# Performance work log

Measured on AMD Instinct MI355X. Metric: run time of the kernel, lower is better.

Reference implementation:

```python
import jax, jax.numpy as jnp
import numpy as np

PI = 3.1415927410125732
N = 4096
L = 1.28e-3          # box side [m]
VEL = 5e-7
RC = 3.15e-6         # Rc = diameter/2
RR = 8e-6
RO = 2.5e-5
RA = np.inf
DT_TRANS = 1.4e-14   # DT (translational diffusion)
DR = 0.0028
GAMMA = 25.0
DT = 0.2             # timestep dt
COLL_ITERS = 30      # fixed cap for collision-resolution do-while (orig caps at 1000)


def setup_inputs() -> dict:
    key = jax.random.key(0)
    ks = jax.random.split(key, 7)
    pos_re = jax.random.uniform(ks[0], (N,), jnp.float32) * L
    pos_im = jax.random.uniform(ks[1], (N,), jnp.float32) * L
    ang = jax.random.uniform(ks[2], (N,), jnp.float32, -PI, PI)
    ori_re = jnp.cos(ang)
    ori_im = jnp.sin(ang)
    deltas = jax.random.uniform(ks[3], (N,), jnp.float32) * 0.5
    rot_noise = jax.random.normal(ks[4], (N,), jnp.float32)
    tn_re = jax.random.normal(ks[5], (N,), jnp.float32)
    tn_im = jax.random.normal(ks[6], (N,), jnp.float32)
    return {"pos_re": pos_re, "pos_im": pos_im, "ori_re": ori_re, "ori_im": ori_im,
            "deltas": deltas, "rot_noise": rot_noise, "tn_re": tn_re, "tn_im": tn_im}


def _wrap(diff):
    # torch get_anglediff wrap: (-2pi,2pi) -> ~(-pi,pi)
    diff = jnp.where(diff <= -PI, jnp.mod(diff, PI), diff)
    return diff - (diff >= PI).astype(diff.dtype) * (2.0 * PI)


def _anglediff(a, b):
    return _wrap(jnp.angle(a) - jnp.angle(b))


def _cossim(a, b):
    # nn.CosineSimilarity(dim=1, eps=1e-14) on view_as_real vectors
    dot = a.real * b.real + a.imag * b.imag
    na = jnp.maximum(jnp.abs(a), 1e-14)
    nb = jnp.maximum(jnp.abs(b), 1e-14)
    return dot / (na * nb)


def _mvc(W, z):
    # real [n,n] mask @ complex [n] vector
    return W @ z.real + 1j * (W @ z.imag)


def _solve_collisions(pos):
    n = pos.shape[0]
    eye_f = jnp.eye(n, dtype=jnp.float32)
    eye_c = eye_f.astype(pos.dtype)

    def step(p):
        diff = p[None, :] - p[:, None] + eye_c  # [i,j] = pos_j - pos_i; diag dummy 1 (nan-safe)
        absd = jnp.abs(diff)
        coll = absd <= (2.0 * RC - eye_f)       # diag threshold negative -> self excluded
        move = jnp.where(coll, diff / jnp.where(coll, absd, 1.0) * ((2.1 * RC - absd) * 0.5), 0.0)
        return p - move.sum(axis=1), coll.sum()

    def body(carry, _):
        p, cont = carry
        p_new, ncoll = step(p)
        p = jnp.where(cont, p_new, p)           # do-while: apply move, then continue if collisions
        return (p, jnp.logical_and(cont, ncoll > 0)), None

    body = jax.checkpoint(body)
    (pos, _), _ = jax.lax.scan(body, (pos, jnp.array(True)), None, length=COLL_ITERS)
    return pos


def _forward(pos_re, pos_im, ori_re, ori_im, deltas, rot_noise, tn_re, tn_im):
    pos = (pos_re + 1j * pos_im).astype(jnp.complex64)
    ori = (ori_re + 1j * ori_im).astype(jnp.complex64)
    n = pos.shape[0]
    eye_b = jnp.eye(n, dtype=bool)

    # pairwise |pos_i - pos_j|; diag made 1 to keep abs() grad-safe (diag is masked out / re-added below)
    dists = jnp.abs(pos[:, None] - pos[None, :] + jnp.eye(n, dtype=pos.dtype))
    mask_rr = (dists <= RR) & ~eye_b              # repulsion zone, self excluded (eye subtracted in orig)
    mask_ro = (dists <= RO + RC) | eye_b          # orientation zone, self included (diag dist 0 in orig)
    mask_ra = (dists <= RA + RC) | eye_b          # Ra = inf -> all ones

    # alpha == 2*pi exactly -> within_view branch skipped (matches original)
    ang = jnp.angle(ori)
    abs_ad = jnp.abs(_wrap(ang[:, None] - ang[None, :]))
    in_front = abs_ad < PI / 2

    Wrr = (mask_rr & in_front).astype(jnp.float32)
    Wro = mask_ro.astype(jnp.float32)
    Wra = mask_ra.astype(jnp.float32)

    n_r = Wrr.sum(axis=1)
    S = _mvc(Wrr, pos) / jnp.maximum(n_r, 1.0) - pos * jnp.sign(n_r)
    d = -S

    n_a = Wra.sum(axis=1)
    cms = _mvc(Wra, pos) / jnp.maximum(n_a, 1.0)
    Ps = cms - pos * jnp.sign(n_a)

    osum = _mvc(Wro, ori)
    left = Ps * jnp.exp(1j * deltas)
    right = Ps * jnp.exp(-1j * deltas)

    # T (=300) >= T_release (=200): choose best turn by cosine similarity
    best = jnp.where(_cossim(left, osum) >= _cossim(right, osum), left, right)

    has_rep = jnp.abs(d) > 0.0
    d_safe = jnp.where(has_rep, d, jnp.ones_like(d))
    att = jnp.where(has_rep, _anglediff(d_safe, ori), _anglediff(best, ori))

    s2dr = np.float32(np.sqrt(2.0 * DR))
    sdt = np.float32(np.sqrt(DT))
    rot = jnp.exp(1j * (DT * GAMMA * DR * jnp.sin(att) + rot_noise * s2dr * sdt))

    # complex standard normal: real/imag each N(0, 1/sqrt(2))
    tnoise = (tn_re + 1j * tn_im) * np.float32(np.sqrt(0.5)) * np.float32(np.sqrt(2.0 * DT_TRANS))
    trans = DT * VEL * ori + tnoise * sdt

    new_pos = _solve_collisions(pos + trans)
    new_ori = ori * rot

    c2r = lambda z: jnp.stack([z.real, z.imag], axis=-1)
    # [5, N, 2]: positions, orientations, orientation_sums, leftturns, rightturns (real views)
    return jnp.stack([c2r(new_pos), c2r(new_ori), c2r(osum), c2r(left), c2r(right)], axis=0)


def reference(pos_re, pos_im, ori_re, ori_im, deltas, rot_noise, tn_re, tn_im):
    return _forward(pos_re, pos_im, ori_re, ori_im, deltas, rot_noise, tn_re, tn_im)
```

## Files before the change

kernel.cpp:

```cpp
#include <hip/hip_runtime.h>

#define NPART 4096
#define PI_F 3.1415927410125732f
#define TWO_PI_F 6.2831854820251465f
#define SENT 4096

__device__ __forceinline__ float wrapf(float d) {
    if (d <= -PI_F) {
        d = fmodf(d, PI_F);
        if (d < 0.0f) d += PI_F;
    }
    if (d >= PI_F) d -= TWO_PI_F;
    return d;
}

__global__ __launch_bounds__(512)
void k_interact(const float* __restrict__ pr, const float* __restrict__ pim,
                const float* __restrict__ orr, const float* __restrict__ oim,
                const float* __restrict__ deltas,
                const float* __restrict__ rot_noise,
                const float* __restrict__ tn_re, const float* __restrict__ tn_im,
                float* __restrict__ out,
                uint2* __restrict__ recQuad, int* __restrict__ recC,
                unsigned short* __restrict__ recNbr16) {
    constexpr float RR_F  = 8e-6f;
    constexpr float RR2   = RR_F * RR_F;
    constexpr float ROC_F = (float)(2.5e-5 + 3.15e-6);
    constexpr float ROC2  = ROC_F * ROC_F;
    constexpr float CUT_F = 14.3e-6f;
    constexpr float CUT2  = CUT_F * CUT_F;

    __shared__ float2 lsP[512];
    __shared__ float2 lsO[512];
    __shared__ float rA0[512], rA1[512], rA2[512], rA3[512], rA4[512];
    __shared__ float rB0[512], rB1[512], rB2[512], rB3[512], rB4[512];
    __shared__ float cr_[512], ci_[512];
    __shared__ int ncnt[16];
    __shared__ unsigned short nbrL[16 * 16];

    int tid = threadIdx.x;
    int li = tid & 7, sl = tid >> 3;
    int i0 = blockIdx.x * 16 + li;
    int i1 = i0 + 8;

    if (tid < 16) ncnt[tid] = 0;

    float pxA = pr[i0], pyA = pim[i0], oxA = orr[i0], oyA = oim[i0];
    float pxB = pr[i1], pyB = pim[i1], oxB = orr[i1], oyB = oim[i1];

    float nAr = 0.0f, SAre = 0.0f, SAim = 0.0f, oAre = 0.0f, oAim = 0.0f;
    float nBr = 0.0f, SBre = 0.0f, SBim = 0.0f, oBre = 0.0f, oBim = 0.0f;
    float cs_re = 0.0f, cs_im = 0.0f;

    for (int c = 0; c < 8; ++c) {
        int j0 = c * 512;
        __syncthreads();
        float jr = pr[j0 + tid], ji = pim[j0 + tid];
        lsP[tid] = make_float2(jr, ji);
        lsO[tid] = make_float2(orr[j0 + tid], oim[j0 + tid]);
        cs_re += jr; cs_im += ji;
        __syncthreads();
#pragma unroll
        for (int t = 0; t < 8; ++t) {
            int jj = sl * 8 + ((t + sl) & 7);
            int j = j0 + jj;
            float2 pv = lsP[jj];
            float drA = pxA - pv.x, diA = pyA - pv.y;
            float d2A = drA * drA + diA * diA;
            float drB = pxB - pv.x, diB = pyB - pv.y;
            float d2B = drB * drB + diB * diB;
            if (__any((d2A <= ROC2) | (d2B <= ROC2))) {
                float2 ov = lsO[jj];
                if (d2A <= ROC2) { oAre += ov.x; oAim += ov.y; }
                float dotA = oxA * ov.x + oyA * ov.y;
                if ((d2A <= RR2) & (dotA > 0.0f) & (j != i0)) {
                    nAr += 1.0f; SAre += pv.x; SAim += pv.y;
                }
                if (d2A <= CUT2 && j != i0) {
                    int slot = atomicAdd(&ncnt[li], 1);
                    if (slot < 16) nbrL[li * 16 + slot] = (unsigned short)j;
                }
                if (d2B <= ROC2) { oBre += ov.x; oBim += ov.y; }
                float dotB = oxB * ov.x + oyB * ov.y;
                if ((d2B <= RR2) & (dotB > 0.0f) & (j != i1)) {
                    nBr += 1.0f; SBre += pv.x; SBim += pv.y;
                }
                if (d2B <= CUT2 && j != i1) {
                    int slot = atomicAdd(&ncnt[li + 8], 1);
                    if (slot < 16) nbrL[(li + 8) * 16 + slot] = (unsigned short)j;
                }
            }
        }
    }

    rA0[tid] = nAr; rA1[tid] = SAre; rA2[tid] = SAim; rA3[tid] = oAre; rA4[tid] = oAim;
    rB0[tid] = nBr; rB1[tid] = SBre; rB2[tid] = SBim; rB3[tid] = oBre; rB4[tid] = oBim;
    cr_[tid] = cs_re; ci_[tid] = cs_im;
    __syncthreads();
    for (int s = 256; s >= 8; s >>= 1) {
        if (tid < s) {
            rA0[tid] += rA0[tid + s]; rA1[tid] += rA1[tid + s];
            rA2[tid] += rA2[tid + s]; rA3[tid] += rA3[tid + s];
            rA4[tid] += rA4[tid + s];
            rB0[tid] += rB0[tid + s]; rB1[tid] += rB1[tid + s];
            rB2[tid] += rB2[tid + s]; rB3[tid] += rB3[tid + s];
            rB4[tid] += rB4[tid + s];
            cr_[tid] += cr_[tid + s];  ci_[tid] += ci_[tid + s];
        }
        __syncthreads();
    }
    if (tid < 4) { cr_[tid] += cr_[tid + 4]; ci_[tid] += ci_[tid + 4]; }
    __syncthreads();
    if (tid < 2) { cr_[tid] += cr_[tid + 2]; ci_[tid] += ci_[tid + 2]; }
    __syncthreads();
    if (tid == 0) { cr_[0] += cr_[1]; ci_[0] += ci_[1]; }
    __syncthreads();

    if (tid < 16) {
        int i = blockIdx.x * 16 + tid;
        float n_r, S_re, S_im, o_re, o_im, px, py, ox, oy;
        if (tid < 8) {
            n_r = rA0[tid]; S_re = rA1[tid]; S_im = rA2[tid];
            o_re = rA3[tid]; o_im = rA4[tid];
            px = pxA; py = pyA; ox = oxA; oy = oyA;
        } else {
            int g = tid - 8;
            n_r = rB0[g]; S_re = rB1[g]; S_im = rB2[g];
            o_re = rB3[g]; o_im = rB4[g];
            px = pxB; py = pyB; ox = oxB; oy = oyB;
        }

        float maxnr = fmaxf(n_r, 1.0f);
        float sgn = (n_r > 0.0f) ? 1.0f : 0.0f;
        float Sre = S_re / maxnr - px * sgn;
        float Sim = S_im / maxnr - py * sgn;
        float d_re = -Sre, d_im = -Sim;

        float cmsx = cr_[0] * (1.0f / 4096.0f);
        float cmsy = ci_[0] * (1.0f / 4096.0f);
        float Ps_re = cmsx - px;
        float Ps_im = cmsy - py;

        float dl = deltas[i];
        float cd = cosf(dl), sd = sinf(dl);
        float l_re = Ps_re * cd - Ps_im * sd;
        float l_im = Ps_re * sd + Ps_im * cd;
        float r_re = Ps_re * cd + Ps_im * sd;
        float r_im = Ps_im * cd - Ps_re * sd;

        float nb   = fmaxf(hypotf(o_re, o_im), 1e-14f);
        float na_l = fmaxf(hypotf(l_re, l_im), 1e-14f);
        float na_r = fmaxf(hypotf(r_re, r_im), 1e-14f);
        float csl = (l_re * o_re + l_im * o_im) / (na_l * nb);
        float csr = (r_re * o_re + r_im * o_im) / (na_r * nb);
        float b_re = (csl >= csr) ? l_re : r_re;
        float b_im = (csl >= csr) ? l_im : r_im;

        float ai = atan2f(oy, ox);
        bool has_rep = (d_re != 0.0f) || (d_im != 0.0f);
        float att;
        if (has_rep) att = wrapf(atan2f(d_im, d_re) - ai);
        else         att = wrapf(atan2f(b_im, b_re) - ai);

        constexpr float GDD  = (float)(0.2 * 25.0 * 0.0028);
        constexpr float S2DR = 0.07483314773547883f;
        constexpr float SDT  = 0.44721359549995793f;
        float theta = GDD * sinf(att) + (rot_noise[i] * S2DR) * SDT;
        float rr_ = cosf(theta), ri_ = sinf(theta);

        float no_re = ox * rr_ - oy * ri_;
        float no_im = ox * ri_ + oy * rr_;

        constexpr float DTVEL = (float)(0.2 * 5e-7);
        constexpr float C1 = 0.70710678118654752f;
        constexpr float C2 = 1.6733200530681511e-07f;
        float t_re = DTVEL * ox + ((tn_re[i] * C1) * C2) * SDT;
        float t_im = DTVEL * oy + ((tn_im[i] * C1) * C2) * SDT;
        float p0x = px + t_re, p0y = py + t_im;

        float2* o2 = (float2*)out;
        o2[i]            = make_float2(p0x, p0y);
        o2[1 * 4096 + i] = make_float2(no_re, no_im);
        o2[2 * 4096 + i] = make_float2(o_re, o_im);
        o2[3 * 4096 + i] = make_float2(l_re, l_im);
        o2[4 * 4096 + i] = make_float2(r_re, r_im);

        int c = min(ncnt[tid], 16);
        unsigned q0 = (c > 0) ? nbrL[tid * 16 + 0] : (unsigned)SENT;
        unsigned q1 = (c > 1) ? nbrL[tid * 16 + 1] : (unsigned)SENT;
        unsigned q2 = (c > 2) ? nbrL[tid * 16 + 2] : (unsigned)SENT;
        unsigned q3 = (c > 3) ? nbrL[tid * 16 + 3] : (unsigned)SENT;
        recQuad[i] = make_uint2(q0 | (q1 << 16), q2 | (q3 << 16));
        recC[i] = c;
        if (c > 4) {
            int cp = (c + 3) & ~3;
            for (int m = 4; m < cp; ++m)
                recNbr16[i * 16 + m] = (m < c) ? nbrL[tid * 16 + m]
                                               : (unsigned short)SENT;
        }
    }
}

__global__ __launch_bounds__(1024)
void k_coll_all(const uint2* __restrict__ recQuad, const int* __restrict__ recC,
                const unsigned short* __restrict__ recNbr16,
                float* __restrict__ out, int* __restrict__ dbg) {
    constexpr float TWO_RC  = (float)(2.0 * 3.15e-6);
    constexpr float TWO_RC2 = TWO_RC * TWO_RC;
    constexpr float C21RC   = (float)(2.1 * 3.15e-6);

    __shared__ float2 pos[NPART + 2];
    __shared__ __align__(16) unsigned short pool[128 * 16];
    __shared__ int flg[2];
    __shared__ int poolCnt;
    __shared__ unsigned bmp[2][132];

    int tid = threadIdx.x;
    if (tid == 0) {
        pos[SENT] = make_float2(1e9f, 1e9f);
        flg[0] = 0; flg[1] = 0; poolCnt = 0;
    }
    if (tid < 132) { bmp[0][tid] = 0u; bmp[1][tid] = 0u; }

    const float2* o2in = (const float2*)out;
    float myx[4], myy[4];
    int myc[4], myo[4];
    int nq0[4], nq1[4], nq2[4], nq3[4];
    bool pm[4];
#pragma unroll
    for (int s = 0; s < 4; ++s) {
        int i = s * 1024 + tid;
        float2 p = o2in[i];
        myx[s] = p.x; myy[s] = p.y;
        pos[i] = p;
        uint2 q = recQuad[i];
        nq0[s] = q.x & 0xffff; nq1[s] = q.x >> 16;
        nq2[s] = q.y & 0xffff; nq3[s] = q.y >> 16;
        myc[s] = recC[i];
        myo[s] = -1;
        pm[s] = true;
    }
    __syncthreads();

#pragma unroll
    for (int s = 0; s < 4; ++s) {
        if (myc[s] > 4) {
            int r = atomicAdd(&poolCnt, 1);
            if (r < 128) {
                int i = s * 1024 + tid;
                const uint4* src = (const uint4*)&recNbr16[i * 16];
                uint4* dst = (uint4*)&pool[r * 16];
                dst[0] = src[0]; dst[1] = src[1];
                myo[s] = r;
            }
        }
    }
    __syncthreads();

    for (int it = 0; it < 30; ++it) {
        int cur = it & 1, nxt = cur ^ 1;
        if (tid < 132) bmp[nxt][tid] = 0u;

        dbg[(it << 10) + tid] = it;

        float nx[4], ny[4];
        int ncs[4];
#pragma unroll
        for (int s = 0; s < 4; ++s) {
            ncs[s] = 0;
            int c = myc[s];
            if (c > 0) {
                bool dirty;
                if (it == 0 || c > 4) {
                    dirty = true;
                } else {
                    unsigned hit = pm[s] ? 1u : 0u;
                    hit |= (bmp[cur][nq0[s] >> 5] >> (nq0[s] & 31)) & 1u;
                    hit |= (bmp[cur][nq1[s] >> 5] >> (nq1[s] & 31)) & 1u;
                    hit |= (bmp[cur][nq2[s] >> 5] >> (nq2[s] & 31)) & 1u;
                    hit |= (bmp[cur][nq3[s] >> 5] >> (nq3[s] & 31)) & 1u;
                    dirty = hit != 0u;
                }
                if (dirty) {
                    float px = myx[s], py = myy[s];
                    float mre = 0.0f, mim = 0.0f;
                    int nc = 0;
                    float2 q0 = pos[nq0[s]], q1 = pos[nq1[s]];
                    float2 q2 = pos[nq2[s]], q3 = pos[nq3[s]];
#define COLL_ONE(q)                                                     \
                    {                                                   \
                        float dr = (q).x - px, di = (q).y - py;         \
                        float d2 = dr * dr + di * di;                   \
                        if (d2 <= TWO_RC2) {                            \
                            float a = sqrtf(d2);                        \
                            float mm = (C21RC - a) * 0.5f / a;          \
                            mre += dr * mm; mim += di * mm; ++nc;       \
                        }                                               \
                    }
                    COLL_ONE(q0) COLL_ONE(q1) COLL_ONE(q2) COLL_ONE(q3)
                    for (int m0 = 4; m0 < c; m0 += 4) {
                        uint2 w;
                        if (myo[s] >= 0)
                            w = *(const uint2*)&pool[myo[s] * 16 + m0];
                        else
                            w = *(const uint2*)&recNbr16[(s * 1024 + tid) * 16 + m0];
                        int j0 = w.x & 0xffff, j1 = w.x >> 16;
                        int j2 = w.y & 0xffff, j3 = w.y >> 16;
                        float2 t0 = pos[j0], t1 = pos[j1], t2 = pos[j2], t3 = pos[j3];
                        COLL_ONE(t0) COLL_ONE(t1) COLL_ONE(t2) COLL_ONE(t3)
                    }
#undef COLL_ONE
                    ncs[s] = nc;
                    nx[s] = px - mre; ny[s] = py - mim;
                }
            }
        }
        __syncthreads();
#pragma unroll
        for (int s = 0; s < 4; ++s) {
            pm[s] = (ncs[s] > 0);
            if (ncs[s] > 0) {
                int i = s * 1024 + tid;
                myx[s] = nx[s]; myy[s] = ny[s];
                pos[i] = make_float2(nx[s], ny[s]);
                atomicOr(&bmp[nxt][i >> 5], 1u << (i & 31));
            }
        }
        int any = ncs[0] | ncs[1] | ncs[2] | ncs[3];
        if (any) flg[it & 1] = 1;
        if (tid == 0) flg[(it + 1) & 1] = 0;
        __syncthreads();
        if (flg[it & 1] == 0) break;
    }

    float2* o2 = (float2*)out;
#pragma unroll
    for (int s = 0; s < 4; ++s)
        o2[s * 1024 + tid] = make_float2(myx[s], myy[s]);
}

extern "C" void kernel_launch(void* const* d_in, const int* in_sizes, int n_in,
                              void* d_out, int out_size, void* d_ws, size_t ws_size,
                              hipStream_t stream) {
    const float* pos_re = (const float*)d_in[0];
    const float* pos_im = (const float*)d_in[1];
    const float* ori_re = (const float*)d_in[2];
    const float* ori_im = (const float*)d_in[3];
    const float* deltas = (const float*)d_in[4];
    const float* rot_noise = (const float*)d_in[5];
    const float* tn_re = (const float*)d_in[6];
    const float* tn_im = (const float*)d_in[7];
    float* out = (float*)d_out;

    uint2* recQuad = (uint2*)d_ws;
    int* recC = (int*)(recQuad + NPART);
    unsigned short* recNbr16 = (unsigned short*)(recC + NPART);
    int* dbg = (int*)(recNbr16 + NPART * 16);

    k_interact<<<256, 512, 0, stream>>>(pos_re, pos_im, ori_re, ori_im,
                                        deltas, rot_noise, tn_re, tn_im,
                                        out, recQuad, recC, recNbr16);
    k_coll_all<<<1, 1024, 0, stream>>>(recQuad, recC, recNbr16, out, dbg);
}
```

Before: 120.1 us.

## Double-buffer collision positions to drop one barrier per iteration

The collision loop now keeps positions in two shared buffers and rotates the dirty bitmaps and continue flags across three slots. Each iteration reads from one buffer and writes to the other, so only one __syncthreads is needed per iteration instead of two. Particles that moved in the previous iteration also rewrite their position into the new buffer so the two buffers stay consistent. The cost is double the shared memory for positions, which may limit occupancy, and the convergence check is deferred to the start of the next iteration.

Result: slower. 124.1 us (+3.4%).

```diff
diff --git a/kernel.cpp b/kernel.cpp
--- a/kernel.cpp
+++ b/kernel.cpp
@@ -209,18 +209,22 @@
     constexpr float TWO_RC2 = TWO_RC * TWO_RC;
     constexpr float C21RC   = (float)(2.1 * 3.15e-6);
 
-    __shared__ float2 pos[NPART + 2];
+    __shared__ float2 pos[2][NPART + 2];
     __shared__ __align__(16) unsigned short pool[128 * 16];
-    __shared__ int flg[2];
     __shared__ int poolCnt;
-    __shared__ unsigned bmp[2][132];
+    __shared__ unsigned bmp3[3][132];
+    __shared__ int flg3[3];
 
     int tid = threadIdx.x;
     if (tid == 0) {
-        pos[SENT] = make_float2(1e9f, 1e9f);
-        flg[0] = 0; flg[1] = 0; poolCnt = 0;
-    }
-    if (tid < 132) { bmp[0][tid] = 0u; bmp[1][tid] = 0u; }
+        pos[0][SENT] = make_float2(1e9f, 1e9f);
+        pos[1][SENT] = make_float2(1e9f, 1e9f);
+        poolCnt = 0;
+        flg3[0] = 0; flg3[1] = 0; flg3[2] = 0;
+    }
+    if (tid < 132) {
+        bmp3[0][tid] = 0u; bmp3[1][tid] = 0u; bmp3[2][tid] = 0u;
+    }
 
     const float2* o2in = (const float2*)out;
     float myx[4], myy[4];
@@ -232,13 +236,13 @@
         int i = s * 1024 + tid;
         float2 p = o2in[i];
         myx[s] = p.x; myy[s] = p.y;
-        pos[i] = p;
+        pos[0][i] = p; pos[1][i] = p;
         uint2 q = recQuad[i];
         nq0[s] = q.x & 0xffff; nq1[s] = q.x >> 16;
         nq2[s] = q.y & 0xffff; nq3[s] = q.y >> 16;
         myc[s] = recC[i];
         myo[s] = -1;
-        pm[s] = true;
+        pm[s] = false;
     }
     __syncthreads();
 
@@ -258,8 +262,11 @@
     __syncthreads();
 
     for (int it = 0; it < 30; ++it) {
-        int cur = it & 1, nxt = cur ^ 1;
-        if (tid < 132) bmp[nxt][tid] = 0u;
+        if (it > 0 && flg3[it % 3] == 0) break;
+        int cb = it & 1, nb = cb ^ 1;
+        int probeS = it % 3, setS = (it + 1) % 3, clrS = (it + 2) % 3;
+        if (tid < 132) bmp3[clrS][tid] = 0u;
+        if (tid == 0) flg3[clrS] = 0;
 
         dbg[(it << 10) + tid] = it;
 
@@ -275,18 +282,18 @@
                     dirty = true;
                 } else {
                     unsigned hit = pm[s] ? 1u : 0u;
-                    hit |= (bmp[cur][nq0[s] >> 5] >> (nq0[s] & 31)) & 1u;
-                    hit |= (bmp[cur][nq1[s] >> 5] >> (nq1[s] & 31)) & 1u;
-                    hit |= (bmp[cur][nq2[s] >> 5] >> (nq2[s] & 31)) & 1u;
-                    hit |= (bmp[cur][nq3[s] >> 5] >> (nq3[s] & 31)) & 1u;
+                    hit |= (bmp3[probeS][nq0[s] >> 5] >> (nq0[s] & 31)) & 1u;
+                    hit |= (bmp3[probeS][nq1[s] >> 5] >> (nq1[s] & 31)) & 1u;
+                    hit |= (bmp3[probeS][nq2[s] >> 5] >> (nq2[s] & 31)) & 1u;
+                    hit |= (bmp3[probeS][nq3[s] >> 5] >> (nq3[s] & 31)) & 1u;
                     dirty = hit != 0u;
                 }
                 if (dirty) {
                     float px = myx[s], py = myy[s];
                     float mre = 0.0f, mim = 0.0f;
                     int nc = 0;
-                    float2 q0 = pos[nq0[s]], q1 = pos[nq1[s]];
-                    float2 q2 = pos[nq2[s]], q3 = pos[nq3[s]];
+                    float2 q0 = pos[cb][nq0[s]], q1 = pos[cb][nq1[s]];
+                    float2 q2 = pos[cb][nq2[s]], q3 = pos[cb][nq3[s]];
 #define COLL_ONE(q)                                                     \
                     {                                                   \
                         float dr = (q).x - px, di = (q).y - py;         \
@@ -306,7 +313,8 @@
                             w = *(const uint2*)&recNbr16[(s * 1024 + tid) * 16 + m0];
                         int j0 = w.x & 0xffff, j1 = w.x >> 16;
                         int j2 = w.y & 0xffff, j3 = w.y >> 16;
-                        float2 t0 = pos[j0], t1 = pos[j1], t2 = pos[j2], t3 = pos[j3];
+                        float2 t0 = pos[cb][j0], t1 = pos[cb][j1];
+                        float2 t2 = pos[cb][j2], t3 = pos[cb][j3];
                         COLL_ONE(t0) COLL_ONE(t1) COLL_ONE(t2) COLL_ONE(t3)
                     }
 #undef COLL_ONE
@@ -315,22 +323,24 @@
                 }
             }
         }
+        int any = 0;
+#pragma unroll
+        for (int s = 0; s < 4; ++s) {
+            bool moved = (ncs[s] > 0);
+            if (moved) { myx[s] = nx[s]; myy[s] = ny[s]; }
+            if (moved || pm[s]) {
+                int i = s * 1024 + tid;
+                pos[nb][i] = make_float2(myx[s], myy[s]);
+            }
+            if (moved) {
+                int i = s * 1024 + tid;
+                atomicOr(&bmp3[setS][i >> 5], 1u << (i & 31));
+            }
+            pm[s] = moved;
+            any |= ncs[s];
+        }
+        if (any) flg3[setS] = 1;
         __syncthreads();
-#pragma unroll
-        for (int s = 0; s < 4; ++s) {
-            pm[s] = (ncs[s] > 0);
-            if (ncs[s] > 0) {
-                int i = s * 1024 + tid;
-                myx[s] = nx[s]; myy[s] = ny[s];
-                pos[i] = make_float2(nx[s], ny[s]);
-                atomicOr(&bmp[nxt][i >> 5], 1u << (i & 31));
-            }
-        }
-        int any = ncs[0] | ncs[1] | ncs[2] | ncs[3];
-        if (any) flg[it & 1] = 1;
-        if (tid == 0) flg[(it + 1) & 1] = 0;
-        __syncthreads();
-        if (flg[it & 1] == 0) break;
     }
 
     float2* o2 = (float2*)out;
```
